# Kernel optimization log

Hardware: AMD Instinct MI355X
Metric: run time of the kernel (lower is better)

The kernel has to match this reference:

```python
import jax, jax.numpy as jnp
import numpy as np

B = 2048
NUM_ITER = 3  # dynamic routing iterations


def _conv2d(x, w, b, pad):
    # x: [B,C,H,W], w: [O,I,kh,kw] (OIHW)
    y = jax.lax.conv_general_dilated(
        x, w, window_strides=(1, 1), padding=[(pad, pad), (pad, pad)],
        dimension_numbers=('NCHW', 'OIHW', 'NCHW'))
    return y + b[None, :, None, None]


def _maxpool2(x):
    return jax.lax.reduce_window(x, -jnp.inf, jax.lax.max,
                                 (1, 1, 2, 2), (1, 1, 2, 2), 'VALID')


def _squash(t, axis=-1):
    # scale = |t|^2/(1+|t|^2); out = scale * t / |t|
    n2 = jnp.sum(t * t, axis=axis, keepdims=True)
    return (n2 / (1.0 + n2)) * t * jax.lax.rsqrt(n2)


def setup_inputs() -> dict:
    key = jax.random.key(0)
    ks = jax.random.split(key, 8)
    f32 = jnp.float32
    rn = lambda k, s, sc=1.0: jax.random.normal(k, s, f32) * sc
    return {
        'x': rn(ks[0], (B, 1, 36, 60)),
        'y': rn(ks[1], (B, 2)),
        'conv1_w': rn(ks[2], (20, 1, 5, 5), 0.1),
        'conv1_b': jnp.zeros((20,), f32),
        'conv2_w': rn(ks[3], (50, 20, 5, 5), 0.01),
        'conv2_b': jnp.zeros((50,), f32),
        'pcaps_w': rn(ks[4], (16, 50, 5, 5), 0.05),   # 4 capsules x 4 out-ch, stacked
        'pcaps_b': jnp.zeros((16,), f32),
        'route_w': rn(ks[5], (2, 288, 4, 1)),          # [num_caps, route_nodes, in_ch, out_ch]
        'fc1_w': rn(ks[6], (500, 3602), 0.02),
        'fc1_b': jnp.zeros((500,), f32),
        'fc2_w': rn(ks[7], (2, 502), 0.05),
        'fc2_b': jnp.zeros((2,), f32),
    }


def reference(x, y, conv1_w, conv1_b, conv2_w, conv2_b, pcaps_w, pcaps_b,
              route_w, fc1_w, fc1_b, fc2_w, fc2_b):
    b = x.shape[0]
    # conv backbone
    h = _maxpool2(_conv2d(x, conv1_w, conv1_b, 0))   # [B,20,16,28]
    h = _maxpool2(_conv2d(h, conv2_w, conv2_b, 0))   # [B,50,6,12]

    # primary capsules: 4 parallel convs (stacked into one), each [B,4,6,12]
    p = _conv2d(h, pcaps_w, pcaps_b, 2)              # [B,16,6,12]
    u = p.reshape(b, 4, 4 * 6 * 12)                  # [B, caps=4, nodes=288] (c,h,w flatten per capsule)
    u = u.transpose(0, 2, 1)                         # [B,288,4]
    u = _squash(u, axis=-1)

    # digit capsules: dynamic routing
    # priors[k,b,r,o] = sum_c u[b,r,c] * W[k,r,c,o]
    priors = jnp.einsum('brc,krco->kbro', u, route_w)  # [2,B,288,1]
    logits = jnp.zeros_like(priors)
    v = None
    for i in range(NUM_ITER):
        probs = jax.nn.softmax(logits, axis=2)
        v = _squash(jnp.sum(probs * priors, axis=2, keepdims=True), axis=-1)  # [2,B,1,1]
        if i < NUM_ITER - 1:
            logits = logits + jnp.sum(priors * v, axis=-1, keepdims=True)

    c = v[:, :, 0, :].transpose(1, 0, 2).reshape(b, -1)  # [B,2]
    xf = h.reshape(b, -1)                                # [B,3600]
    f = jnp.concatenate([xf, c], axis=-1)                # [B,3602]
    f = jax.nn.relu(f @ fc1_w.T + fc1_b)                 # [B,500]
    f = jnp.concatenate([f, y], axis=1)                  # [B,502]
    return f @ fc2_w.T + fc2_b                           # [B,2]
```

## Files before the change

kernel.cpp:

```cpp
#include <hip/hip_runtime.h>
#include <math.h>


#define BATCH 2048

typedef __attribute__((ext_vector_type(8))) short short8;
typedef __attribute__((ext_vector_type(4))) float floatx4;
typedef unsigned short u16;
typedef unsigned int   u32;

__device__ inline float wave_sum(float v) {
#pragma unroll
    for (int off = 32; off >= 1; off >>= 1) v += __shfl_xor(v, off);
    return v;
}
__device__ inline float wave_max(float v) {
#pragma unroll
    for (int off = 32; off >= 1; off >>= 1) v = fmaxf(v, __shfl_xor(v, off));
    return v;
}
__device__ inline u16 f2bf(float f) {
    u32 u = __float_as_uint(f);
    u32 r = (u + 0x7FFFu + ((u >> 16) & 1u)) >> 16;
    return (u16)r;
}

__global__ __launch_bounds__(256) void k_wconv(const float* __restrict__ fw,
                                               u16* __restrict__ w_bf) {
    int g  = blockIdx.x * 256 + threadIdx.x;
    int n  = (g * 8) / 3616;
    int k0 = (g * 8) % 3616;
    u16 v[8];
#pragma unroll
    for (int j = 0; j < 8; ++j) {
        int kk = k0 + j;
        float f = 0.f;
        if (n < 500 && kk < 3600) {
            int pos = kk / 50;
            int oc  = kk - 50 * pos;
            f = fw[(size_t)n * 3602 + oc * 72 + pos];
        }
        v[j] = f2bf(f);
    }
    *(short8*)&w_bf[(size_t)g * 8] = *(short8*)v;
}

__global__ __launch_bounds__(256) void k_w2conv(const float* __restrict__ w2,
                                                u16* __restrict__ w2t) {
    int g = blockIdx.x * 256 + threadIdx.x;
    if (g >= 6400) return;
    int idx = g * 8;
    int tap = idx >> 11;
    int oc  = (idx >> 5) & 63;
    int ic0 = idx & 31;
    u16 v[8];
#pragma unroll
    for (int j = 0; j < 8; ++j) {
        int ic = ic0 + j;
        float f = (ic < 20 && oc < 50) ? w2[oc * 500 + ic * 25 + tap] : 0.f;
        v[j] = f2bf(f);
    }
    *(short8*)&w2t[idx] = *(short8*)v;
}

__global__ __launch_bounds__(256) void k_pwconv(const float* __restrict__ pcw,
                                                u16* __restrict__ w_pc) {
    int g = blockIdx.x * 256 + threadIdx.x;
    if (g >= 3200) return;
    int idx = g * 8;
    int tap = idx >> 10;
    int rem = idx & 1023;
    int oc  = rem >> 6;
    int ic0 = rem & 63;
    u16 v[8];
#pragma unroll
    for (int j = 0; j < 8; ++j) {
        int ic = ic0 + j;
        float f = (ic < 50) ? pcw[(oc * 50 + ic) * 25 + tap] : 0.f;
        v[j] = f2bf(f);
    }
    *(short8*)&w_pc[idx] = *(short8*)v;
}

__global__ __launch_bounds__(256, 3) void k_convs(
    const float* __restrict__ x, const float* __restrict__ w1,
    const float* __restrict__ b1, const u16* __restrict__ w2t,
    const float* __restrict__ b2, u32* __restrict__ h_bf)
{
    __shared__ __align__(16) u16 h1t[17920];
    __shared__ __align__(16) float sbuf[2732];
    float* xs  = sbuf;
    float* w1s = sbuf + 2232;

    const int t = threadIdx.x;
    const int b = blockIdx.x;

    for (int i = t; i < 2688; i += 256) {
        int pos = i / 6, c = i - 6 * pos;
        ((u32*)h1t)[pos * 20 + 10 + c] = 0u;
    }
    const float* xb = x + b * 2160;
    for (int i = t; i < 2160; i += 256) {
        int r = i / 60, c = i - 60 * r;
        xs[r * 62 + c] = xb[i];
    }
    for (int i = t; i < 500; i += 256) w1s[i] = w1[i];
    __syncthreads();

#pragma unroll 1
    for (int u = t; u < 1280; u += 256) {
        int oc = u % 20;
        int g  = u / 20;
        int xg = g & 3;
        int y  = g >> 2;
        float wv[25];
#pragma unroll
        for (int j = 0; j < 25; ++j) wv[j] = w1s[oc * 25 + j];
        float acc[7][4];
#pragma unroll
        for (int p = 0; p < 7; ++p)
#pragma unroll
            for (int qq = 0; qq < 4; ++qq) acc[p][qq] = 0.f;
#pragma unroll
        for (int r = 0; r < 6; ++r) {
            float row[18];
            const float* src = &xs[(2 * y + r) * 62 + 14 * xg];
#pragma unroll
            for (int k = 0; k < 9; ++k) {
                float2 v = *(const float2*)&src[2 * k];
                row[2 * k] = v.x; row[2 * k + 1] = v.y;
            }
#pragma unroll
            for (int p = 0; p < 7; ++p)
#pragma unroll
                for (int s = 0; s < 5; ++s) {
                    float x0 = row[2 * p + s], x1 = row[2 * p + 1 + s];
                    if (r < 5) {
                        float w = wv[r * 5 + s];
                        acc[p][0] += x0 * w; acc[p][1] += x1 * w;
                    }
                    if (r >= 1) {
                        float w = wv[(r - 1) * 5 + s];
                        acc[p][2] += x0 * w; acc[p][3] += x1 * w;
                    }
                }
        }
        float bias = b1[oc];
#pragma unroll
        for (int p = 0; p < 7; ++p) {
            float v = bias + fmaxf(fmaxf(acc[p][0], acc[p][1]),
                                   fmaxf(acc[p][2], acc[p][3]));
            h1t[(y * 28 + 7 * xg + p) * 40 + oc] = f2bf(v);
        }
    }
    __syncthreads();

    const int lane = t & 63, w = t >> 6;
    const int r16  = lane & 15;
    const int q    = lane >> 4;
    int abase[5];
#pragma unroll
    for (int i = 0; i < 5; ++i) {
        int mt = w + 4 * i;
        if (mt < 18) {
            int m  = mt * 16 + r16;
            int pq = m >> 2, sub = m & 3;
            int py = pq / 12, px = pq - py * 12;
            int yy = py * 2 + (sub >> 1);
            int xx = px * 2 + (sub & 1);
            abase[i] = (yy * 28 + xx) * 40 + q * 8;
        } else abase[i] = 0;
    }
    floatx4 acc2[5][4] = {};
    const u16* wtb = w2t + r16 * 32 + q * 8;

    short8 bf[4];
#pragma unroll
    for (int nt = 0; nt < 4; ++nt)
        bf[nt] = *(const short8*)&wtb[nt * 512];

#pragma unroll 1
    for (int tap = 0; tap < 25; ++tap) {
        short8 bfn[4];
        if (tap < 24) {
#pragma unroll
            for (int nt = 0; nt < 4; ++nt)
                bfn[nt] = *(const short8*)&wtb[(tap + 1) * 2048 + nt * 512];
        }
        int r = tap / 5, s = tap - 5 * r;
        int aoff = r * 1120 + s * 40;
#pragma unroll
        for (int i = 0; i < 5; ++i) {
            int mt = w + 4 * i;
            if (mt < 18) {
                short8 af = *(const short8*)&h1t[abase[i] + aoff];
#pragma unroll
                for (int nt = 0; nt < 4; ++nt)
                    acc2[i][nt] = __builtin_amdgcn_mfma_f32_16x16x32_bf16(
                        af, bf[nt], acc2[i][nt], 0, 0, 0);
            }
        }
#pragma unroll
        for (int nt = 0; nt < 4; ++nt) bf[nt] = bfn[nt];
    }
    __syncthreads();

    float* hs2 = (float*)h1t;
#pragma unroll
    for (int i = 0; i < 5; ++i) {
        int mt = w + 4 * i;
        if (mt < 18) {
            int pq = mt * 4 + q;
#pragma unroll
            for (int nt = 0; nt < 4; ++nt) {
                int oc = nt * 16 + r16;
                if (oc < 50) {
                    floatx4 a = acc2[i][nt];
                    float v = fmaxf(fmaxf(a[0], a[1]), fmaxf(a[2], a[3])) + b2[oc];
                    hs2[pq * 50 + oc] = v;
                }
            }
        }
    }
    __syncthreads();
    u32* ho = h_bf + (size_t)b * 1808;
    for (int i = t; i < 1808; i += 256) {
        int i2 = 2 * i;
        u32 lo = (i2 < 3600) ? f2bf(hs2[i2]) : 0u;
        u32 hi = (i2 + 1 < 3600) ? f2bf(hs2[i2 + 1]) : 0u;
        ho[i] = lo | (hi << 16);
    }
}

__global__ __launch_bounds__(256) void k_pcaps(
    const u32* __restrict__ h_bf, const u16* __restrict__ w_pc,
    const float* __restrict__ pcb, const float* __restrict__ rw,
    float* __restrict__ cbuf)
{
    __shared__ __align__(16) u16 hsbuf[12672];
    __shared__ __align__(16) float pri[576];
    const int t = threadIdx.x;
    const int b = blockIdx.x;

    for (int i = t; i < 6336; i += 256) ((u32*)hsbuf)[i] = 0u;
    __syncthreads();
    {
        const u32* hb = h_bf + (size_t)b * 1808;
        for (int i = t; i < 1800; i += 256) {
            u32 v   = hb[i];
            int k2  = 2 * i;
            int pos = k2 / 50;
            int oc  = k2 - 50 * pos;
            int ph  = pos / 12, pw = pos - 12 * ph;
            ((u32*)hsbuf)[((((ph + 2) * 16) + pw + 2) * 72 + oc) >> 1] = v;
        }
    }
    __syncthreads();

    const int lane = t & 63, w = t >> 6;
    const int r16  = lane & 15;
    const int q    = lane >> 4;
    int abase[5];
#pragma unroll
    for (int mt = 0; mt < 5; ++mt) {
        int m  = mt * 16 + r16;
        int ph = m / 12, pw = m - 12 * ph;
        abase[mt] = (ph * 16 + pw) * 72 + q * 8;
    }
    floatx4 acc[5] = {};
    const u16* wp = w_pc + r16 * 64 + q * 8;
    const int ntap = (28 - w) >> 2;
#pragma unroll 1
    for (int tt = 0; tt < ntap; ++tt) {
        int tap = w + 4 * tt;
        short8 b0 = *(const short8*)&wp[tap * 1024];
        short8 b1 = *(const short8*)&wp[tap * 1024 + 32];
        int r = tap / 5, s = tap - 5 * r;
        int aoff = (r * 16 + s) * 72;
#pragma unroll
        for (int mt = 0; mt < 5; ++mt) {
            short8 a0 = *(const short8*)&hsbuf[abase[mt] + aoff];
            short8 a1 = *(const short8*)&hsbuf[abase[mt] + aoff + 32];
            acc[mt] = __builtin_amdgcn_mfma_f32_16x16x32_bf16(a0, b0, acc[mt], 0, 0, 0);
            acc[mt] = __builtin_amdgcn_mfma_f32_16x16x32_bf16(a1, b1, acc[mt], 0, 0, 0);
        }
    }
    __syncthreads();

    float* psum = (float*)hsbuf;
#pragma unroll
    for (int mt = 0; mt < 5; ++mt)
#pragma unroll
        for (int i = 0; i < 4; ++i) {
            int m = mt * 16 + q * 4 + i;
            psum[w * 1280 + m * 16 + r16] = acc[mt][i];
        }
    __syncthreads();

    for (int i = t; i < 1152; i += 256) {
        float s = psum[i] + psum[1280 + i] + psum[2560 + i] + psum[3840 + i]
                + pcb[i & 15];
        psum[i] = s;
    }
    __syncthreads();

    for (int r = t; r < 288; r += 256) {
        int sub = r / 72;
        int pos = r - sub * 72;
        float u0 = psum[pos * 16 + 0  + sub];
        float u1 = psum[pos * 16 + 4  + sub];
        float u2 = psum[pos * 16 + 8  + sub];
        float u3 = psum[pos * 16 + 12 + sub];
        float n2 = u0 * u0 + u1 * u1 + u2 * u2 + u3 * u3;
        float scale = (n2 / (1.0f + n2)) * rsqrtf(n2);
        u0 *= scale; u1 *= scale; u2 *= scale; u3 *= scale;
#pragma unroll
        for (int k = 0; k < 2; ++k) {
            const float4 wv = *(const float4*)&rw[(k * 288 + r) * 4];
            pri[k * 288 + r] = u0 * wv.x + u1 * wv.y + u2 * wv.z + u3 * wv.w;
        }
    }
    __syncthreads();

    if (w < 2) {
        const float* pr = &pri[w * 288];
        float p[5];
        bool  val[5];
#pragma unroll
        for (int j = 0; j < 5; ++j) {
            int r  = j * 64 + lane;
            val[j] = r < 288;
            p[j]   = val[j] ? pr[r] : 0.0f;
        }
        float tot = wave_sum(p[0] + p[1] + p[2] + p[3] + p[4]);
        float s = tot * (1.0f / 288.0f);
        float a = s * fabsf(s) / (1.0f + s * s);
#pragma unroll
        for (int it = 0; it < 2; ++it) {
            float l[5];
            float lm = -INFINITY;
#pragma unroll
            for (int j = 0; j < 5; ++j) {
                l[j] = val[j] ? p[j] * a : -INFINITY;
                lm   = fmaxf(lm, l[j]);
            }
            lm = wave_max(lm);
            float se = 0.f, sp = 0.f;
#pragma unroll
            for (int j = 0; j < 5; ++j) {
                float e = val[j] ? expf(l[j] - lm) : 0.f;
                se += e;
                sp += e * p[j];
            }
            se = wave_sum(se);
            sp = wave_sum(sp);
            float sv = sp / se;
            float v  = sv * fabsf(sv) / (1.0f + sv * sv);
            if (it == 0) a += v;
            else if (lane == 0) cbuf[b * 2 + w] = v;
        }
    }
}

__global__ __launch_bounds__(256) void k_fc1(
    const u16* __restrict__ h_bf, const u16* __restrict__ w_bf,
    const float* __restrict__ cc, const float* __restrict__ w,
    const float* __restrict__ bias, float* __restrict__ f1)
{
    __shared__ __align__(16) u16 As[64 * 40];
    __shared__ __align__(16) u16 Bs[64 * 40];
    const int t  = threadIdx.x;
    const int m0 = blockIdx.x * 64;
    const int n0 = blockIdx.y * 64;
    const int row = t >> 2, c8 = (t & 3) * 8;
    const u16* ha = &h_bf[(size_t)(m0 + row) * 3616 + c8];
    const u16* wa = &w_bf[(size_t)(n0 + row) * 3616 + c8];
    short8 areg = *(const short8*)ha;
    short8 breg = *(const short8*)wa;
    const int lane = t & 63, wv = t >> 6;
    const int r16 = lane & 15, q = lane >> 4;
    const int wr = row * 40 + (t & 3) * 8;
    const int ar = (wv * 16 + r16) * 40 + q * 8;
    const int br = r16 * 40 + q * 8;
    floatx4 acc[4] = {};
#pragma unroll 1
    for (int it = 0; it < 113; ++it) {
        __syncthreads();
        *(short8*)&As[wr] = areg;
        *(short8*)&Bs[wr] = breg;
        __syncthreads();
        if (it < 112) {
            areg = *(const short8*)(ha + (it + 1) * 32);
            breg = *(const short8*)(wa + (it + 1) * 32);
        }
        short8 af = *(const short8*)&As[ar];
#pragma unroll
        for (int nt = 0; nt < 4; ++nt) {
            short8 bf = *(const short8*)&Bs[nt * 640 + br];
            acc[nt] = __builtin_amdgcn_mfma_f32_16x16x32_bf16(af, bf, acc[nt], 0, 0, 0);
        }
    }
    const int mbase = m0 + wv * 16 + q * 4;
#pragma unroll
    for (int nt = 0; nt < 4; ++nt) {
        int n = n0 + nt * 16 + r16;
        if (n < 500) {
            float bn  = bias[n];
            float wc0 = w[(size_t)n * 3602 + 3600];
            float wc1 = w[(size_t)n * 3602 + 3601];
#pragma unroll
            for (int i = 0; i < 4; ++i) {
                int m = mbase + i;
                float v = acc[nt][i] + bn + cc[m * 2] * wc0 + cc[m * 2 + 1] * wc1;
                f1[(size_t)m * 500 + n] = fmaxf(v, 0.f);
            }
        }
    }
}

__global__ __launch_bounds__(256) void k_fc2(
    const float* __restrict__ f1, const float* __restrict__ y,
    const float* __restrict__ w, const float* __restrict__ bias,
    float* __restrict__ out)
{
    int wg   = blockIdx.x * 4 + (threadIdx.x >> 6);
    int lane = threadIdx.x & 63;
    int b = wg >> 1, j = wg & 1;
    const float* wj = w + j * 502;
    float acc = 0.f;
    for (int k = lane; k < 500; k += 64) acc += f1[(size_t)b * 500 + k] * wj[k];
    if (lane < 2) acc += y[b * 2 + lane] * wj[500 + lane];
    acc = wave_sum(acc);
    if (lane == 0) out[b * 2 + j] = acc + bias[j];
}

extern "C" void kernel_launch(void* const* d_in, const int* in_sizes, int n_in,
                              void* d_out, int out_size, void* d_ws, size_t ws_size,
                              hipStream_t stream) {
    const float* x    = (const float*)d_in[0];
    const float* y    = (const float*)d_in[1];
    const float* c1w  = (const float*)d_in[2];
    const float* c1b  = (const float*)d_in[3];
    const float* c2w  = (const float*)d_in[4];
    const float* c2b  = (const float*)d_in[5];
    const float* pcw  = (const float*)d_in[6];
    const float* pcb  = (const float*)d_in[7];
    const float* rw   = (const float*)d_in[8];
    const float* f1w  = (const float*)d_in[9];
    const float* f1b  = (const float*)d_in[10];
    const float* f2w  = (const float*)d_in[11];
    const float* f2b  = (const float*)d_in[12];
    float* out = (float*)d_out;

    u32*   h_bf   = (u32*)d_ws;
    u16*   w_bf   = (u16*)(h_bf + (size_t)BATCH * 1808);
    u16*   w2t    = w_bf + (size_t)512 * 3616;
    u16*   w_pc   = w2t + 51200;
    float* cbuf   = (float*)(w_pc + 25600);
    float* f1     = cbuf + BATCH * 2;

    k_wconv<<<904, 256, 0, stream>>>(f1w, w_bf);
    k_w2conv<<<25, 256, 0, stream>>>(c2w, w2t);
    k_pwconv<<<13, 256, 0, stream>>>(pcw, w_pc);
    k_convs<<<BATCH, 256, 0, stream>>>(x, c1w, c1b, w2t, c2b, h_bf);
    k_pcaps<<<BATCH, 256, 0, stream>>>(h_bf, w_pc, pcb, rw, cbuf);
    dim3 g4(32, 8);
    k_fc1<<<g4, 256, 0, stream>>>((const u16*)h_bf, w_bf, cbuf, f1w, f1b, f1);
    k_fc2<<<BATCH * 2 / 4, 256, 0, stream>>>(f1, y, f2w, f2b, out);
}
```

Baseline: 279.6 us.

## Run conv1 as bf16 MFMA via per-row im2col; merge weight prep kernels

Replaces the scalar FP32 5x5 conv1 with an im2col approach. Each conv output row pair is unpacked into a 25-tap (padded to 32) bf16 patch matrix in shared memory and multiplied on MFMA 16x16x32 against a prepacked bf16 conv1 weight tile. The 2x2 max-pool is folded into the MFMA accumulator layout. The three weight-conversion launches plus a new conv1 weight pack are merged into one prep kernel, removing launch overhead. Input is now rounded to bf16 before conv1, which lowers precision, and the per-row loop adds two barriers per iteration.

```diff
diff --git a/kernel.cpp b/kernel.cpp
--- a/kernel.cpp
+++ b/kernel.cpp
@@ -25,72 +25,84 @@
     return (u16)r;
 }
 
-__global__ __launch_bounds__(256) void k_wconv(const float* __restrict__ fw,
-                                               u16* __restrict__ w_bf) {
-    int g  = blockIdx.x * 256 + threadIdx.x;
-    int n  = (g * 8) / 3616;
-    int k0 = (g * 8) % 3616;
-    u16 v[8];
-#pragma unroll
-    for (int j = 0; j < 8; ++j) {
-        int kk = k0 + j;
-        float f = 0.f;
-        if (n < 500 && kk < 3600) {
-            int pos = kk / 50;
-            int oc  = kk - 50 * pos;
-            f = fw[(size_t)n * 3602 + oc * 72 + pos];
-        }
-        v[j] = f2bf(f);
-    }
-    *(short8*)&w_bf[(size_t)g * 8] = *(short8*)v;
-}
-
-__global__ __launch_bounds__(256) void k_w2conv(const float* __restrict__ w2,
-                                                u16* __restrict__ w2t) {
-    int g = blockIdx.x * 256 + threadIdx.x;
-    if (g >= 6400) return;
-    int idx = g * 8;
-    int tap = idx >> 11;
-    int oc  = (idx >> 5) & 63;
-    int ic0 = idx & 31;
-    u16 v[8];
-#pragma unroll
-    for (int j = 0; j < 8; ++j) {
-        int ic = ic0 + j;
-        float f = (ic < 20 && oc < 50) ? w2[oc * 500 + ic * 25 + tap] : 0.f;
-        v[j] = f2bf(f);
-    }
-    *(short8*)&w2t[idx] = *(short8*)v;
-}
-
-__global__ __launch_bounds__(256) void k_pwconv(const float* __restrict__ pcw,
-                                                u16* __restrict__ w_pc) {
-    int g = blockIdx.x * 256 + threadIdx.x;
-    if (g >= 3200) return;
-    int idx = g * 8;
-    int tap = idx >> 10;
-    int rem = idx & 1023;
-    int oc  = rem >> 6;
-    int ic0 = rem & 63;
-    u16 v[8];
-#pragma unroll
-    for (int j = 0; j < 8; ++j) {
-        int ic = ic0 + j;
-        float f = (ic < 50) ? pcw[(oc * 50 + ic) * 25 + tap] : 0.f;
-        v[j] = f2bf(f);
-    }
-    *(short8*)&w_pc[idx] = *(short8*)v;
+__global__ __launch_bounds__(256) void k_prep(
+    const float* __restrict__ fw,  u16* __restrict__ w_bf,
+    const float* __restrict__ w2,  u16* __restrict__ w2t,
+    const float* __restrict__ pcw, u16* __restrict__ w_pc,
+    const float* __restrict__ w1,  u16* __restrict__ w1t)
+{
+    const int blk = blockIdx.x, t = threadIdx.x;
+    if (blk < 904) {
+        int g  = blk * 256 + t;
+        int n  = (g * 8) / 3616;
+        int k0 = (g * 8) % 3616;
+        u16 v[8];
+#pragma unroll
+        for (int j = 0; j < 8; ++j) {
+            int kk = k0 + j;
+            float f = 0.f;
+            if (n < 500 && kk < 3600) {
+                int pos = kk / 50;
+                int oc  = kk - 50 * pos;
+                f = fw[(size_t)n * 3602 + oc * 72 + pos];
+            }
+            v[j] = f2bf(f);
+        }
+        *(short8*)&w_bf[(size_t)g * 8] = *(short8*)v;
+    } else if (blk < 929) {
+        int g   = (blk - 904) * 256 + t;
+        int idx = g * 8;
+        int tap = idx >> 11;
+        int oc  = (idx >> 5) & 63;
+        int ic0 = idx & 31;
+        u16 v[8];
+#pragma unroll
+        for (int j = 0; j < 8; ++j) {
+            int ic = ic0 + j;
+            float f = (ic < 20 && oc < 50) ? w2[oc * 500 + ic * 25 + tap] : 0.f;
+            v[j] = f2bf(f);
+        }
+        *(short8*)&w2t[idx] = *(short8*)v;
+    } else if (blk < 942) {
+        int g = (blk - 929) * 256 + t;
+        if (g >= 3200) return;
+        int idx = g * 8;
+        int tap = idx >> 10;
+        int rem = idx & 1023;
+        int oc  = rem >> 6;
+        int ic0 = rem & 63;
+        u16 v[8];
+#pragma unroll
+        for (int j = 0; j < 8; ++j) {
+            int ic = ic0 + j;
+            float f = (ic < 50) ? pcw[(oc * 50 + ic) * 25 + tap] : 0.f;
+            v[j] = f2bf(f);
+        }
+        *(short8*)&w_pc[idx] = *(short8*)v;
+    } else {
+        if (t < 128) {
+            int n  = t >> 2;
+            int k0 = (t & 3) * 8;
+            u16 v[8];
+#pragma unroll
+            for (int j = 0; j < 8; ++j) {
+                int k = k0 + j;
+                float f = (n < 20 && k < 25) ? w1[n * 25 + k] : 0.f;
+                v[j] = f2bf(f);
+            }
+            *(short8*)&w1t[t * 8] = *(short8*)v;
+        }
+    }
 }
 
 __global__ __launch_bounds__(256, 3) void k_convs(
-    const float* __restrict__ x, const float* __restrict__ w1,
+    const float* __restrict__ x, const u16* __restrict__ w1t,
     const float* __restrict__ b1, const u16* __restrict__ w2t,
     const float* __restrict__ b2, u32* __restrict__ h_bf)
 {
     __shared__ __align__(16) u16 h1t[17920];
-    __shared__ __align__(16) float sbuf[2732];
-    float* xs  = sbuf;
-    float* w1s = sbuf + 2232;
+    __shared__ __align__(16) u16 xbf[2304];
+    __shared__ __align__(16) u16 im2[4480];
 
     const int t = threadIdx.x;
     const int b = blockIdx.x;
@@ -102,62 +114,81 @@
     const float* xb = x + b * 2160;
     for (int i = t; i < 2160; i += 256) {
         int r = i / 60, c = i - 60 * r;
-        xs[r * 62 + c] = xb[i];
-    }
-    for (int i = t; i < 500; i += 256) w1s[i] = w1[i];
-    __syncthreads();
-
-#pragma unroll 1
-    for (int u = t; u < 1280; u += 256) {
-        int oc = u % 20;
-        int g  = u / 20;
-        int xg = g & 3;
-        int y  = g >> 2;
-        float wv[25];
-#pragma unroll
-        for (int j = 0; j < 25; ++j) wv[j] = w1s[oc * 25 + j];
-        float acc[7][4];
-#pragma unroll
-        for (int p = 0; p < 7; ++p)
-#pragma unroll
-            for (int qq = 0; qq < 4; ++qq) acc[p][qq] = 0.f;
-#pragma unroll
-        for (int r = 0; r < 6; ++r) {
-            float row[18];
-            const float* src = &xs[(2 * y + r) * 62 + 14 * xg];
-#pragma unroll
-            for (int k = 0; k < 9; ++k) {
-                float2 v = *(const float2*)&src[2 * k];
-                row[2 * k] = v.x; row[2 * k + 1] = v.y;
-            }
-#pragma unroll
-            for (int p = 0; p < 7; ++p)
-#pragma unroll
-                for (int s = 0; s < 5; ++s) {
-                    float x0 = row[2 * p + s], x1 = row[2 * p + 1 + s];
-                    if (r < 5) {
-                        float w = wv[r * 5 + s];
-                        acc[p][0] += x0 * w; acc[p][1] += x1 * w;
-                    }
-                    if (r >= 1) {
-                        float w = wv[(r - 1) * 5 + s];
-                        acc[p][2] += x0 * w; acc[p][3] += x1 * w;
-                    }
-                }
-        }
-        float bias = b1[oc];
-#pragma unroll
-        for (int p = 0; p < 7; ++p) {
-            float v = bias + fmaxf(fmaxf(acc[p][0], acc[p][1]),
-                                   fmaxf(acc[p][2], acc[p][3]));
-            h1t[(y * 28 + 7 * xg + p) * 40 + oc] = f2bf(v);
-        }
+        xbf[r * 64 + c] = f2bf(xb[i]);
     }
     __syncthreads();
 
     const int lane = t & 63, w = t >> 6;
     const int r16  = lane & 15;
     const int q    = lane >> 4;
+
+    short8 w1f[2];
+#pragma unroll
+    for (int nt = 0; nt < 2; ++nt)
+        w1f[nt] = *(const short8*)&w1t[(nt * 16 + r16) * 32 + q * 8];
+
+    const int p_   = t;
+    const int px_  = p_ >> 2;
+    const int dy_  = (p_ & 3) >> 1, dx_ = p_ & 1;
+    const int xc_  = 2 * px_ + dx_;
+    const int j0_  = xc_ >> 1;
+    const int par_ = xc_ & 1;
+
+#pragma unroll 1
+    for (int c = 0; c < 16; ++c) {
+        if (t < 112) {
+            u16 tap[25];
+#pragma unroll
+            for (int r = 0; r < 5; ++r) {
+                const u32* U = (const u32*)&xbf[(2 * c + dy_ + r) * 64];
+                u32 A0 = U[j0_], A1 = U[j0_ + 1], A2 = U[j0_ + 2];
+                u16 e0 = par_ ? (u16)(A0 >> 16) : (u16)A0;
+                u16 e1 = par_ ? (u16)A1         : (u16)(A0 >> 16);
+                u16 e2 = par_ ? (u16)(A1 >> 16) : (u16)A1;
+                u16 e3 = par_ ? (u16)A2         : (u16)(A1 >> 16);
+                u16 e4 = par_ ? (u16)(A2 >> 16) : (u16)A2;
+                tap[r * 5 + 0] = e0; tap[r * 5 + 1] = e1; tap[r * 5 + 2] = e2;
+                tap[r * 5 + 3] = e3; tap[r * 5 + 4] = e4;
+            }
+            u32 ow[16];
+#pragma unroll
+            for (int j = 0; j < 12; ++j)
+                ow[j] = (u32)tap[2 * j] | ((u32)tap[2 * j + 1] << 16);
+            ow[12] = (u32)tap[24];
+            ow[13] = 0u; ow[14] = 0u; ow[15] = 0u;
+            u32* dst = (u32*)&im2[p_ * 40];
+            *(uint4*)&dst[0]  = make_uint4(ow[0],  ow[1],  ow[2],  ow[3]);
+            *(uint4*)&dst[4]  = make_uint4(ow[4],  ow[5],  ow[6],  ow[7]);
+            *(uint4*)&dst[8]  = make_uint4(ow[8],  ow[9],  ow[10], ow[11]);
+            *(uint4*)&dst[12] = make_uint4(ow[12], ow[13], ow[14], ow[15]);
+        }
+        __syncthreads();
+#pragma unroll
+        for (int mi = 0; mi < 2; ++mi) {
+            int mt = w + 4 * mi;
+            if (mt < 7) {
+                short8 af = *(const short8*)&im2[(mt * 16 + r16) * 40 + q * 8];
+                floatx4 a1[2] = {};
+#pragma unroll
+                for (int nt = 0; nt < 2; ++nt)
+                    a1[nt] = __builtin_amdgcn_mfma_f32_16x16x32_bf16(
+                        af, w1f[nt], a1[nt], 0, 0, 0);
+                int pq = mt * 4 + q;
+#pragma unroll
+                for (int nt = 0; nt < 2; ++nt) {
+                    int oc = nt * 16 + r16;
+                    if (oc < 20) {
+                        floatx4 a = a1[nt];
+                        float v = fmaxf(fmaxf(a[0], a[1]), fmaxf(a[2], a[3]))
+                                + b1[oc];
+                        h1t[(c * 28 + pq) * 40 + oc] = f2bf(v);
+                    }
+                }
+            }
+        }
+        __syncthreads();
+    }
+
     int abase[5];
 #pragma unroll
     for (int i = 0; i < 5; ++i) {
@@ -396,8 +427,8 @@
         short8 af = *(const short8*)&As[ar];
 #pragma unroll
         for (int nt = 0; nt < 4; ++nt) {
-            short8 bf = *(const short8*)&Bs[nt * 640 + br];
-            acc[nt] = __builtin_amdgcn_mfma_f32_16x16x32_bf16(af, bf, acc[nt], 0, 0, 0);
+            short8 bfv = *(const short8*)&Bs[nt * 640 + br];
+            acc[nt] = __builtin_amdgcn_mfma_f32_16x16x32_bf16(af, bfv, acc[nt], 0, 0, 0);
         }
     }
     const int mbase = m0 + wv * 16 + q * 4;
@@ -456,13 +487,12 @@
     u16*   w_bf   = (u16*)(h_bf + (size_t)BATCH * 1808);
     u16*   w2t    = w_bf + (size_t)512 * 3616;
     u16*   w_pc   = w2t + 51200;
-    float* cbuf   = (float*)(w_pc + 25600);
+    u16*   w1t    = w_pc + 25600;
+    float* cbuf   = (float*)(w1t + 1024);
     float* f1     = cbuf + BATCH * 2;
 
-    k_wconv<<<904, 256, 0, stream>>>(f1w, w_bf);
-    k_w2conv<<<25, 256, 0, stream>>>(c2w, w2t);
-    k_pwconv<<<13, 256, 0, stream>>>(pcw, w_pc);
-    k_convs<<<BATCH, 256, 0, stream>>>(x, c1w, c1b, w2t, c2b, h_bf);
+    k_prep<<<943, 256, 0, stream>>>(f1w, w_bf, c2w, w2t, pcw, w_pc, c1w, w1t);
+    k_convs<<<BATCH, 256, 0, stream>>>(x, w1t, c1b, w2t, c2b, h_bf);
     k_pcaps<<<BATCH, 256, 0, stream>>>(h_bf, w_pc, pcb, rw, cbuf);
     dim3 g4(32, 8);
     k_fc1<<<g4, 256, 0, stream>>>((const u16*)h_bf, w_bf, cbuf, f1w, f1b, f1);
```

Result: faster. 271.1 us (-3.0%).
